# Optimization experiments

Measured on AMD Instinct MI355X. Metric: run time of the kernel, lower is better.

## Reference

```python
import jax, jax.numpy as jnp
import numpy as np

B, T, DIM, HID = 8, 2048, 1024, 128

def setup_inputs() -> dict:
    key = jax.random.key(0)
    ks = jax.random.split(key, 6)
    x = jax.random.normal(ks[0], (B, T, DIM), dtype=jnp.float32)
    wk_w = jax.random.normal(ks[1], (DIM, HID), dtype=jnp.float32) * 0.02
    wk_b = jnp.zeros((HID,), dtype=jnp.float32)
    wv_w = jax.random.normal(ks[2], (DIM, HID), dtype=jnp.float32) * 0.02
    wv_b = jnp.zeros((HID,), dtype=jnp.float32)
    # xavier_uniform for w [T,T]: bound = sqrt(6/(T+T))
    bound = float(np.sqrt(6.0 / (T + T)))
    w = jax.random.uniform(ks[3], (T, T), dtype=jnp.float32, minval=-bound, maxval=bound)
    return {"x": x, "wk_w": wk_w, "wk_b": wk_b, "wv_w": wv_w, "wv_b": wv_b, "w": w}

def reference(x, wk_w, wk_b, wv_w, wv_b, w):
    # K, V projections: [B,T,HID]
    K = x @ wk_w + wk_b
    V = x @ wv_w + wv_b
    eK = jnp.exp(K)            # [B,T,HID]
    ew = jnp.exp(w)            # [T,T], shared left operand of both matmuls
    num = jnp.einsum('ts,bsh->bth', ew, eK * V)  # exp(w) @ (exp(K)*V)
    den = jnp.einsum('ts,bsh->bth', ew, eK)      # exp(w) @ exp(K)
    # Original module returns `weighted` (before sigmoid(Q) gating and ffnn)
    return num / den
```

## Files before the change

### kernel.cpp

```cpp
#include <hip/hip_runtime.h>
#include <hip/hip_bf16.h>


#define T_    2048
#define DIM_  1024
#define HID_  128

typedef __attribute__((ext_vector_type(8))) __bf16 bf16x8;
typedef __attribute__((ext_vector_type(4))) float f32x4;
typedef __attribute__((ext_vector_type(4))) unsigned short us4;
typedef __attribute__((ext_vector_type(8))) unsigned short us8;

typedef const unsigned int __attribute__((address_space(1)))* gas_t;
typedef unsigned int __attribute__((address_space(3)))* las_t;

__device__ __forceinline__ unsigned short f2bf(float f) {
    unsigned int u = __builtin_bit_cast(unsigned int, f);
    u += 0x7fffu + ((u >> 16) & 1u);
    return (unsigned short)(u >> 16);
}

__device__ __forceinline__ void gload16(const void* g, void* l) {
    __builtin_amdgcn_global_load_lds((gas_t)g, (las_t)l, 16, 0, 0);
}

__global__ __launch_bounds__(256) void prep_ew(const float* __restrict__ w,
                                               unsigned short* __restrict__ ew) {
    int idx = blockIdx.x * 256 + threadIdx.x;
    f32x4 v = ((const f32x4*)w)[idx];
    us4 o;
    o[0] = f2bf(__expf(v[0]));
    o[1] = f2bf(__expf(v[1]));
    o[2] = f2bf(__expf(v[2]));
    o[3] = f2bf(__expf(v[3]));
    ((us4*)ew)[idx] = o;
}

__global__ __launch_bounds__(256) void prep_wkv(const float* __restrict__ wk,
                                                const float* __restrict__ wv,
                                                unsigned short* __restrict__ wkvT) {
    int t = blockIdx.x * 256 + threadIdx.x;
    int n = t & 255, k0 = (t >> 8) << 3;
    const float* src = (n < 128) ? (wk + n) : (wv + (n - 128));
    us8 o;
#pragma unroll
    for (int j = 0; j < 8; j++) o[j] = f2bf(src[(size_t)(k0 + j) * 128]);
    *(us8*)(&wkvT[n * 1024 + k0]) = o;
}

__global__ __launch_bounds__(256) void gemm1(const float* __restrict__ x,
                                             const unsigned short* __restrict__ wkvT,
                                             const float* __restrict__ wk_b,
                                             const float* __restrict__ wv_b,
                                             unsigned short* __restrict__ KVc) {
    __shared__ __align__(16) unsigned short As[2][32 * 72];
    __shared__ __align__(16) unsigned short Bs[2][256 * 64];
    const int tid  = threadIdx.x;
    const int m0   = blockIdx.x * 32;
    const int bb   = m0 >> 11;
    const int t0   = m0 & (T_ - 1);
    const int wave = tid >> 6, lane = tid & 63;
    const int lr = lane & 15, lq = lane >> 4;

    f32x4 acc[2][4];
#pragma unroll
    for (int i = 0; i < 2; i++)
#pragma unroll
        for (int j = 0; j < 4; j++) acc[i][j] = {0.f, 0.f, 0.f, 0.f};

    f32x4 aC[2], aN[2];
#pragma unroll
    for (int i = 0; i < 2; i++) {
        int c = i * 256 + tid, r = c >> 4, c4 = (c & 15) * 4;
        aC[i] = *(const f32x4*)(x + (size_t)(m0 + r) * DIM_ + c4);
    }
#pragma unroll
    for (int i = 0; i < 8; i++) {
        int c = i * 256 + tid, r = c >> 3, kc = ((c & 7) ^ (r & 7)) * 8;
        gload16(wkvT + (size_t)r * DIM_ + kc, &Bs[0][(i * 256 + wave * 64) * 8]);
    }

    int cur = 0;
    for (int t = 0; t < 16; t++) {
        if (t < 15) {
            int k0 = (t + 1) * 64;
#pragma unroll
            for (int i = 0; i < 2; i++) {
                int c = i * 256 + tid, r = c >> 4, c4 = (c & 15) * 4;
                aN[i] = *(const f32x4*)(x + (size_t)(m0 + r) * DIM_ + k0 + c4);
            }
#pragma unroll
            for (int i = 0; i < 8; i++) {
                int c = i * 256 + tid, r = c >> 3, kc = ((c & 7) ^ (r & 7)) * 8;
                gload16(wkvT + (size_t)r * DIM_ + k0 + kc,
                        &Bs[cur ^ 1][(i * 256 + wave * 64) * 8]);
            }
            asm volatile("s_waitcnt vmcnt(10)" ::: "memory");
        } else {
            asm volatile("s_waitcnt vmcnt(0)" ::: "memory");
        }
#pragma unroll
        for (int i = 0; i < 2; i++) {
            int c = i * 256 + tid, r = c >> 4, c4 = (c & 15) * 4;
            us4 o;
            o[0] = f2bf(aC[i][0]); o[1] = f2bf(aC[i][1]);
            o[2] = f2bf(aC[i][2]); o[3] = f2bf(aC[i][3]);
            *(us4*)(&As[cur][r * 72 + c4]) = o;
        }
        asm volatile("s_waitcnt lgkmcnt(0)" ::: "memory");
        __builtin_amdgcn_s_barrier();
#pragma unroll
        for (int ks = 0; ks < 64; ks += 32) {
            bf16x8 af[2], bfr[4];
#pragma unroll
            for (int mf = 0; mf < 2; mf++)
                af[mf] = *(const bf16x8*)(&As[cur][(mf * 16 + lr) * 72 + ks + lq * 8]);
#pragma unroll
            for (int nf = 0; nf < 4; nf++) {
                int rb = (nf < 2) ? (wave * 32 + nf * 16 + lr)
                                  : (128 + wave * 32 + (nf - 2) * 16 + lr);
                bfr[nf] = *(const bf16x8*)(&Bs[cur][rb * 64 + ((ks + lq * 8) ^ ((rb & 7) << 3))]);
            }
#pragma unroll
            for (int mf = 0; mf < 2; mf++)
#pragma unroll
                for (int nf = 0; nf < 4; nf++)
                    acc[mf][nf] = __builtin_amdgcn_mfma_f32_16x16x32_bf16(
                        af[mf], bfr[nf], acc[mf][nf], 0, 0, 0);
        }
        __builtin_amdgcn_s_barrier();
        aC[0] = aN[0]; aC[1] = aN[1];
        cur ^= 1;
    }

    unsigned short* ekvS = &Bs[0][0];
    unsigned short* ekS  = ekvS + 128 * 40;
#pragma unroll
    for (int nf = 0; nf < 2; nf++) {
        int h = wave * 32 + nf * 16 + lr;
        float bk = wk_b[h], bv = wv_b[h];
#pragma unroll
        for (int mf = 0; mf < 2; mf++) {
            int m = mf * 16 + lq * 4;
            us4 ok, okv;
#pragma unroll
            for (int j = 0; j < 4; j++) {
                float ek = __expf(acc[mf][nf][j] + bk);
                float vv = acc[mf][nf + 2][j] + bv;
                ok[j]  = f2bf(ek);
                okv[j] = f2bf(ek * vv);
            }
            *(us4*)(ekS  + h * 40 + m) = ok;
            *(us4*)(ekvS + h * 40 + m) = okv;
        }
    }
    __syncthreads();
    unsigned short* dst = KVc + (size_t)bb * 256 * T_;
#pragma unroll
    for (int i = 0; i < 2; i++) {
        int c = i * 256 + tid;
        int h = c >> 2, mc = (c & 3) * 8;
        us8 vkv = *(const us8*)(ekvS + h * 40 + mc);
        us8 vk  = *(const us8*)(ekS  + h * 40 + mc);
        *(us8*)(dst + (size_t)h * T_ + t0 + mc)         = vkv;
        *(us8*)(dst + (size_t)(128 + h) * T_ + t0 + mc) = vk;
    }
}

__global__ __launch_bounds__(256) void gemm2(const unsigned short* __restrict__ ew,
                                             const unsigned short* __restrict__ KVc,
                                             float* __restrict__ out) {
    __shared__ __align__(16) unsigned short As[2][32 * 64];
    __shared__ __align__(16) unsigned short Bs[2][256 * 64];
    const int tid  = threadIdx.x;
    const int t0   = blockIdx.x * 32;
    const int b    = blockIdx.y;
    const unsigned short* Bsrc = KVc + (size_t)b * 256 * T_;
    const int wave = tid >> 6, lane = tid & 63;
    const int lr = lane & 15, lq = lane >> 4;

    f32x4 acc[2][4];
#pragma unroll
    for (int i = 0; i < 2; i++)
#pragma unroll
        for (int j = 0; j < 4; j++) acc[i][j] = {0.f, 0.f, 0.f, 0.f};

#define STAGE2(BUF, K0) do {                                                      \
    { int c = tid, r = c >> 3, kc = ((c & 7) ^ (r & 7)) * 8;                      \
      gload16(ew + (size_t)(t0 + r) * T_ + (K0) + kc, &As[BUF][(wave * 64) * 8]); } \
    _Pragma("unroll")                                                             \
    for (int i = 0; i < 8; i++) {                                                 \
        int c = i * 256 + tid, r = c >> 3, kc = ((c & 7) ^ (r & 7)) * 8;          \
        gload16(Bsrc + (size_t)r * T_ + (K0) + kc,                                \
                &Bs[BUF][(i * 256 + wave * 64) * 8]);                             \
    } } while (0)

    STAGE2(0, 0);

    int cur = 0;
    for (int t = 0; t < 32; t++) {
        if (t < 31) {
            STAGE2(cur ^ 1, (t + 1) * 64);
            asm volatile("s_waitcnt vmcnt(9)" ::: "memory");
        } else {
            asm volatile("s_waitcnt vmcnt(0)" ::: "memory");
        }
        __builtin_amdgcn_s_barrier();
#pragma unroll
        for (int ks = 0; ks < 64; ks += 32) {
            bf16x8 af[2], bfr[4];
#pragma unroll
            for (int mf = 0; mf < 2; mf++) {
                int ra = mf * 16 + lr;
                af[mf] = *(const bf16x8*)(&As[cur][ra * 64 + ((ks + lq * 8) ^ ((ra & 7) << 3))]);
            }
#pragma unroll
            for (int nf = 0; nf < 4; nf++) {
                int rb = (nf < 2) ? (wave * 32 + nf * 16 + lr)
                                  : (128 + wave * 32 + (nf - 2) * 16 + lr);
                bfr[nf] = *(const bf16x8*)(&Bs[cur][rb * 64 + ((ks + lq * 8) ^ ((rb & 7) << 3))]);
            }
#pragma unroll
            for (int mf = 0; mf < 2; mf++)
#pragma unroll
                for (int nf = 0; nf < 4; nf++)
                    acc[mf][nf] = __builtin_amdgcn_mfma_f32_16x16x32_bf16(
                        af[mf], bfr[nf], acc[mf][nf], 0, 0, 0);
        }
        __builtin_amdgcn_s_barrier();
        cur ^= 1;
    }
#undef STAGE2

    float* ob = out + ((size_t)b * T_ + t0) * HID_;
#pragma unroll
    for (int nf = 0; nf < 2; nf++) {
        int h = wave * 32 + nf * 16 + lr;
#pragma unroll
        for (int mf = 0; mf < 2; mf++) {
            int m = mf * 16 + lq * 4;
#pragma unroll
            for (int j = 0; j < 4; j++)
                ob[(size_t)(m + j) * HID_ + h] = acc[mf][nf][j] / acc[mf][nf + 2][j];
        }
    }
}

extern "C" void kernel_launch(void* const* d_in, const int* in_sizes, int n_in,
                              void* d_out, int out_size, void* d_ws, size_t ws_size,
                              hipStream_t stream) {
    const float* x    = (const float*)d_in[0];
    const float* wk_w = (const float*)d_in[1];
    const float* wk_b = (const float*)d_in[2];
    const float* wv_w = (const float*)d_in[3];
    const float* wv_b = (const float*)d_in[4];
    const float* w    = (const float*)d_in[5];

    char* ws = (char*)d_ws;
    unsigned short* ws_ew   = (unsigned short*)(ws);
    unsigned short* ws_wkvT = (unsigned short*)(ws + (8u << 20));
    unsigned short* ws_KVc  = (unsigned short*)(ws + (9u << 20));

    prep_ew  <<<4096, 256, 0, stream>>>(w, ws_ew);
    prep_wkv <<<128,  256, 0, stream>>>(wk_w, wv_w, ws_wkvT);
    gemm1    <<<512,  256, 0, stream>>>(x, ws_wkvT, wk_b, wv_b, ws_KVc);
    gemm2    <<<dim3(64, 8), 256, 0, stream>>>(ws_ew, ws_KVc, (float*)d_out);
}
```

Measured before the change: 165.6 us.

## Enlarge GEMM M-tile to 64 rows with 512-thread blocks and swizzled A tile

Both GEMM kernels now use 64-row M tiles with 8 waves per block instead of 32 rows and 4 waves. Each wave computes 4x2 MFMA fragments, and the shared B tile (the 256-wide weight or KV panel) is reused across twice as many rows. This halves B traffic per output. gemm1's A tile switches from padded rows to an XOR swizzle, and gemm2's grid is flattened with the batch index in the low bits so neighbouring blocks share time rows of exp(w). The cost is half as many blocks (256 on a large-CU device), which may leave CUs underused.

```diff
diff --git a/kernel.cpp b/kernel.cpp
--- a/kernel.cpp
+++ b/kernel.cpp
@@ -48,36 +48,36 @@
     *(us8*)(&wkvT[n * 1024 + k0]) = o;
 }
 
-__global__ __launch_bounds__(256) void gemm1(const float* __restrict__ x,
+__global__ __launch_bounds__(512) void gemm1(const float* __restrict__ x,
                                              const unsigned short* __restrict__ wkvT,
                                              const float* __restrict__ wk_b,
                                              const float* __restrict__ wv_b,
                                              unsigned short* __restrict__ KVc) {
-    __shared__ __align__(16) unsigned short As[2][32 * 72];
+    __shared__ __align__(16) unsigned short As[2][64 * 64];
     __shared__ __align__(16) unsigned short Bs[2][256 * 64];
     const int tid  = threadIdx.x;
-    const int m0   = blockIdx.x * 32;
+    const int m0   = blockIdx.x * 64;
     const int bb   = m0 >> 11;
     const int t0   = m0 & (T_ - 1);
     const int wave = tid >> 6, lane = tid & 63;
     const int lr = lane & 15, lq = lane >> 4;
 
-    f32x4 acc[2][4];
-#pragma unroll
-    for (int i = 0; i < 2; i++)
-#pragma unroll
-        for (int j = 0; j < 4; j++) acc[i][j] = {0.f, 0.f, 0.f, 0.f};
+    f32x4 acc[4][2];
+#pragma unroll
+    for (int i = 0; i < 4; i++)
+#pragma unroll
+        for (int j = 0; j < 2; j++) acc[i][j] = {0.f, 0.f, 0.f, 0.f};
 
     f32x4 aC[2], aN[2];
 #pragma unroll
     for (int i = 0; i < 2; i++) {
-        int c = i * 256 + tid, r = c >> 4, c4 = (c & 15) * 4;
+        int c = i * 512 + tid, r = c >> 4, c4 = (c & 15) * 4;
         aC[i] = *(const f32x4*)(x + (size_t)(m0 + r) * DIM_ + c4);
     }
 #pragma unroll
-    for (int i = 0; i < 8; i++) {
-        int c = i * 256 + tid, r = c >> 3, kc = ((c & 7) ^ (r & 7)) * 8;
-        gload16(wkvT + (size_t)r * DIM_ + kc, &Bs[0][(i * 256 + wave * 64) * 8]);
+    for (int i = 0; i < 4; i++) {
+        int c = i * 512 + tid, r = c >> 3, kc = ((c & 7) ^ (r & 7)) * 8;
+        gload16(wkvT + (size_t)r * DIM_ + kc, &Bs[0][(i * 512 + wave * 64) * 8]);
     }
 
     int cur = 0;
@@ -86,45 +86,47 @@
             int k0 = (t + 1) * 64;
 #pragma unroll
             for (int i = 0; i < 2; i++) {
-                int c = i * 256 + tid, r = c >> 4, c4 = (c & 15) * 4;
+                int c = i * 512 + tid, r = c >> 4, c4 = (c & 15) * 4;
                 aN[i] = *(const f32x4*)(x + (size_t)(m0 + r) * DIM_ + k0 + c4);
             }
 #pragma unroll
-            for (int i = 0; i < 8; i++) {
-                int c = i * 256 + tid, r = c >> 3, kc = ((c & 7) ^ (r & 7)) * 8;
+            for (int i = 0; i < 4; i++) {
+                int c = i * 512 + tid, r = c >> 3, kc = ((c & 7) ^ (r & 7)) * 8;
                 gload16(wkvT + (size_t)r * DIM_ + k0 + kc,
-                        &Bs[cur ^ 1][(i * 256 + wave * 64) * 8]);
-            }
-            asm volatile("s_waitcnt vmcnt(10)" ::: "memory");
+                        &Bs[cur ^ 1][(i * 512 + wave * 64) * 8]);
+            }
+            asm volatile("s_waitcnt vmcnt(6)" ::: "memory");
         } else {
             asm volatile("s_waitcnt vmcnt(0)" ::: "memory");
         }
 #pragma unroll
         for (int i = 0; i < 2; i++) {
-            int c = i * 256 + tid, r = c >> 4, c4 = (c & 15) * 4;
+            int c = i * 512 + tid, r = c >> 4, c4 = (c & 15) * 4;
+            int sw = ((((c4 >> 3) ^ (r & 7)) << 3) | (c4 & 7));
             us4 o;
             o[0] = f2bf(aC[i][0]); o[1] = f2bf(aC[i][1]);
             o[2] = f2bf(aC[i][2]); o[3] = f2bf(aC[i][3]);
-            *(us4*)(&As[cur][r * 72 + c4]) = o;
+            *(us4*)(&As[cur][r * 64 + sw]) = o;
         }
         asm volatile("s_waitcnt lgkmcnt(0)" ::: "memory");
         __builtin_amdgcn_s_barrier();
 #pragma unroll
         for (int ks = 0; ks < 64; ks += 32) {
-            bf16x8 af[2], bfr[4];
-#pragma unroll
-            for (int mf = 0; mf < 2; mf++)
-                af[mf] = *(const bf16x8*)(&As[cur][(mf * 16 + lr) * 72 + ks + lq * 8]);
-#pragma unroll
-            for (int nf = 0; nf < 4; nf++) {
-                int rb = (nf < 2) ? (wave * 32 + nf * 16 + lr)
-                                  : (128 + wave * 32 + (nf - 2) * 16 + lr);
+            bf16x8 af[4], bfr[2];
+#pragma unroll
+            for (int mf = 0; mf < 4; mf++) {
+                int ra = mf * 16 + lr;
+                af[mf] = *(const bf16x8*)(&As[cur][ra * 64 + ((ks + lq * 8) ^ ((ra & 7) << 3))]);
+            }
+#pragma unroll
+            for (int nf = 0; nf < 2; nf++) {
+                int rb = nf * 128 + wave * 16 + lr;
                 bfr[nf] = *(const bf16x8*)(&Bs[cur][rb * 64 + ((ks + lq * 8) ^ ((rb & 7) << 3))]);
             }
 #pragma unroll
-            for (int mf = 0; mf < 2; mf++)
-#pragma unroll
-                for (int nf = 0; nf < 4; nf++)
+            for (int mf = 0; mf < 4; mf++)
+#pragma unroll
+                for (int nf = 0; nf < 2; nf++)
                     acc[mf][nf] = __builtin_amdgcn_mfma_f32_16x16x32_bf16(
                         af[mf], bfr[nf], acc[mf][nf], 0, 0, 0);
         }
@@ -134,65 +136,66 @@
     }
 
     unsigned short* ekvS = &Bs[0][0];
-    unsigned short* ekS  = ekvS + 128 * 40;
-#pragma unroll
-    for (int nf = 0; nf < 2; nf++) {
-        int h = wave * 32 + nf * 16 + lr;
+    unsigned short* ekS  = ekvS + 128 * 72;
+    {
+        int h = wave * 16 + lr;
         float bk = wk_b[h], bv = wv_b[h];
 #pragma unroll
-        for (int mf = 0; mf < 2; mf++) {
+        for (int mf = 0; mf < 4; mf++) {
             int m = mf * 16 + lq * 4;
             us4 ok, okv;
 #pragma unroll
             for (int j = 0; j < 4; j++) {
-                float ek = __expf(acc[mf][nf][j] + bk);
-                float vv = acc[mf][nf + 2][j] + bv;
+                float ek = __expf(acc[mf][0][j] + bk);
+                float vv = acc[mf][1][j] + bv;
                 ok[j]  = f2bf(ek);
                 okv[j] = f2bf(ek * vv);
             }
-            *(us4*)(ekS  + h * 40 + m) = ok;
-            *(us4*)(ekvS + h * 40 + m) = okv;
+            *(us4*)(ekS  + h * 72 + m) = ok;
+            *(us4*)(ekvS + h * 72 + m) = okv;
         }
     }
     __syncthreads();
     unsigned short* dst = KVc + (size_t)bb * 256 * T_;
 #pragma unroll
     for (int i = 0; i < 2; i++) {
-        int c = i * 256 + tid;
-        int h = c >> 2, mc = (c & 3) * 8;
-        us8 vkv = *(const us8*)(ekvS + h * 40 + mc);
-        us8 vk  = *(const us8*)(ekS  + h * 40 + mc);
+        int c = i * 512 + tid;
+        int h = c >> 3, mc = (c & 7) * 8;
+        us8 vkv = *(const us8*)(ekvS + h * 72 + mc);
+        us8 vk  = *(const us8*)(ekS  + h * 72 + mc);
         *(us8*)(dst + (size_t)h * T_ + t0 + mc)         = vkv;
         *(us8*)(dst + (size_t)(128 + h) * T_ + t0 + mc) = vk;
     }
 }
 
-__global__ __launch_bounds__(256) void gemm2(const unsigned short* __restrict__ ew,
+__global__ __launch_bounds__(512) void gemm2(const unsigned short* __restrict__ ew,
                                              const unsigned short* __restrict__ KVc,
                                              float* __restrict__ out) {
-    __shared__ __align__(16) unsigned short As[2][32 * 64];
+    __shared__ __align__(16) unsigned short As[2][64 * 64];
     __shared__ __align__(16) unsigned short Bs[2][256 * 64];
     const int tid  = threadIdx.x;
-    const int t0   = blockIdx.x * 32;
-    const int b    = blockIdx.y;
+    const int bid  = blockIdx.x;
+    const int b    = bid & 7;
+    const int t0   = (bid >> 3) * 64;
     const unsigned short* Bsrc = KVc + (size_t)b * 256 * T_;
     const int wave = tid >> 6, lane = tid & 63;
     const int lr = lane & 15, lq = lane >> 4;
 
-    f32x4 acc[2][4];
-#pragma unroll
-    for (int i = 0; i < 2; i++)
-#pragma unroll
-        for (int j = 0; j < 4; j++) acc[i][j] = {0.f, 0.f, 0.f, 0.f};
+    f32x4 acc[4][2];
+#pragma unroll
+    for (int i = 0; i < 4; i++)
+#pragma unroll
+        for (int j = 0; j < 2; j++) acc[i][j] = {0.f, 0.f, 0.f, 0.f};
 
 #define STAGE2(BUF, K0) do {                                                      \
     { int c = tid, r = c >> 3, kc = ((c & 7) ^ (r & 7)) * 8;                      \
-      gload16(ew + (size_t)(t0 + r) * T_ + (K0) + kc, &As[BUF][(wave * 64) * 8]); } \
+      gload16(ew + (size_t)(t0 + r) * T_ + (K0) + kc,                             \
+              &As[BUF][(wave * 64) * 8]); }                                       \
     _Pragma("unroll")                                                             \
-    for (int i = 0; i < 8; i++) {                                                 \
-        int c = i * 256 + tid, r = c >> 3, kc = ((c & 7) ^ (r & 7)) * 8;          \
+    for (int i = 0; i < 4; i++) {                                                 \
+        int c = i * 512 + tid, r = c >> 3, kc = ((c & 7) ^ (r & 7)) * 8;          \
         gload16(Bsrc + (size_t)r * T_ + (K0) + kc,                                \
-                &Bs[BUF][(i * 256 + wave * 64) * 8]);                             \
+                &Bs[BUF][(i * 512 + wave * 64) * 8]);                             \
     } } while (0)
 
     STAGE2(0, 0);
@@ -201,29 +204,28 @@
     for (int t = 0; t < 32; t++) {
         if (t < 31) {
             STAGE2(cur ^ 1, (t + 1) * 64);
-            asm volatile("s_waitcnt vmcnt(9)" ::: "memory");
+            asm volatile("s_waitcnt vmcnt(5)" ::: "memory");
         } else {
             asm volatile("s_waitcnt vmcnt(0)" ::: "memory");
         }
         __builtin_amdgcn_s_barrier();
 #pragma unroll
         for (int ks = 0; ks < 64; ks += 32) {
-            bf16x8 af[2], bfr[4];
-#pragma unroll
-            for (int mf = 0; mf < 2; mf++) {
+            bf16x8 af[4], bfr[2];
+#pragma unroll
+            for (int mf = 0; mf < 4; mf++) {
                 int ra = mf * 16 + lr;
                 af[mf] = *(const bf16x8*)(&As[cur][ra * 64 + ((ks + lq * 8) ^ ((ra & 7) << 3))]);
             }
 #pragma unroll
-            for (int nf = 0; nf < 4; nf++) {
-                int rb = (nf < 2) ? (wave * 32 + nf * 16 + lr)
-                                  : (128 + wave * 32 + (nf - 2) * 16 + lr);
+            for (int nf = 0; nf < 2; nf++) {
+                int rb = nf * 128 + wave * 16 + lr;
                 bfr[nf] = *(const bf16x8*)(&Bs[cur][rb * 64 + ((ks + lq * 8) ^ ((rb & 7) << 3))]);
             }
 #pragma unroll
-            for (int mf = 0; mf < 2; mf++)
-#pragma unroll
-                for (int nf = 0; nf < 4; nf++)
+            for (int mf = 0; mf < 4; mf++)
+#pragma unroll
+                for (int nf = 0; nf < 2; nf++)
                     acc[mf][nf] = __builtin_amdgcn_mfma_f32_16x16x32_bf16(
                         af[mf], bfr[nf], acc[mf][nf], 0, 0, 0);
         }
@@ -233,15 +235,14 @@
 #undef STAGE2
 
     float* ob = out + ((size_t)b * T_ + t0) * HID_;
-#pragma unroll
-    for (int nf = 0; nf < 2; nf++) {
-        int h = wave * 32 + nf * 16 + lr;
-#pragma unroll
-        for (int mf = 0; mf < 2; mf++) {
+    {
+        int h = wave * 16 + lr;
+#pragma unroll
+        for (int mf = 0; mf < 4; mf++) {
             int m = mf * 16 + lq * 4;
 #pragma unroll
             for (int j = 0; j < 4; j++)
-                ob[(size_t)(m + j) * HID_ + h] = acc[mf][nf][j] / acc[mf][nf + 2][j];
+                ob[(size_t)(m + j) * HID_ + h] = acc[mf][0][j] / acc[mf][1][j];
         }
     }
 }
@@ -263,6 +264,6 @@
 
     prep_ew  <<<4096, 256, 0, stream>>>(w, ws_ew);
     prep_wkv <<<128,  256, 0, stream>>>(wk_w, wv_w, ws_wkvT);
-    gemm1    <<<512,  256, 0, stream>>>(x, ws_wkvT, wk_b, wv_b, ws_KVc);
-    gemm2    <<<dim3(64, 8), 256, 0, stream>>>(ws_ew, ws_KVc, (float*)d_out);
-}
+    gemm1    <<<256,  512, 0, stream>>>(x, ws_wkvT, wk_b, wv_b, ws_KVc);
+    gemm2    <<<256,  512, 0, stream>>>(ws_ew, ws_KVc, (float*)d_out);
+}
```

After: 166.3 us. No clear change (+0.4%).
